# Performance work log

Measured on AMD Instinct MI355X. Metric: run time of the kernel, lower is better.

Reference implementation:

```python
import jax, jax.numpy as jnp
import numpy as np

MAX_EMBED = 1024
MAX_HEADS = 16
MIN_WIDTH_RATIO = 0.25


def setup_inputs() -> dict:
    key = jax.random.key(0)
    ks = jax.random.split(key, 10)
    B, S, E = 4, 1024, MAX_EMBED
    query = jax.random.normal(ks[0], (B, S, E), dtype=jnp.float32)
    attention_mask = jax.random.randint(ks[1], (B, 1, 1, S), 0, 2, dtype=jnp.int32)
    # SlimmableLinear params (max sizes); kaiming-ish scale ~ 1/sqrt(fan_in)
    scale = 1.0 / np.sqrt(E)
    def lin(kw, kb):
        w = jax.random.uniform(kw, (E, E), dtype=jnp.float32, minval=-scale, maxval=scale)
        b = jax.random.uniform(kb, (E,), dtype=jnp.float32, minval=-scale, maxval=scale)
        return w, b
    q_w, q_b = lin(ks[2], ks[3])
    k_w, k_b = lin(ks[4], ks[5])
    v_w, v_b = lin(ks[6], ks[7])
    o_w, o_b = lin(ks[8], ks[9])
    return {"query": query, "attention_mask": attention_mask,
            "q_w": q_w, "q_b": q_b, "k_w": k_w, "k_b": k_b,
            "v_w": v_w, "v_b": v_b, "o_w": o_w, "o_b": o_b,
            "width": 768}


def _slim_linear(x, w, b, width):
    # weight stored [out, in] like torch; slice to [width, width]
    return x[..., :width] @ w[:width, :width].T + b[:width]


def reference(query, attention_mask, q_w, q_b, k_w, k_b, v_w, v_b, o_w, o_b, width):
    min_width = int(MAX_EMBED * MIN_WIDTH_RATIO)
    width = max(min_width, min(int(width), MAX_EMBED))
    num_heads = max(1, width * MAX_HEADS // MAX_EMBED)
    head_dim = width // num_heads
    B, S, _ = query.shape

    q = _slim_linear(query, q_w, q_b, width)  # [B,S,width]
    k = _slim_linear(query, k_w, k_b, width)  # key=query (self-attn)
    v = _slim_linear(query, v_w, v_b, width)

    q = q.reshape(B, S, num_heads, head_dim).transpose(0, 2, 1, 3)  # [B,H,S,D]
    k = k.reshape(B, S, num_heads, head_dim).transpose(0, 2, 1, 3)
    v = v.reshape(B, S, num_heads, head_dim).transpose(0, 2, 1, 3)

    scores = jnp.einsum('bhqd,bhkd->bhqk', q, k) / jnp.sqrt(jnp.float32(head_dim))
    scores = jnp.where(attention_mask == 0, jnp.float32(-1e9), scores)
    attn_weights = jax.nn.softmax(scores, axis=-1)  # [B,H,S,S]
    attn_output = jnp.einsum('bhqk,bhkd->bhqd', attn_weights, v)
    attn_output = attn_output.transpose(0, 2, 1, 3).reshape(B, S, width)
    output = attn_output @ o_w[:width, :width].T + o_b[:width]
    return output, attn_weights
```

## Files before the change

### kernel.cpp

```cpp
#include <hip/hip_runtime.h>

#define Bn 4
#define Sn 1024
#define En 1024
#define Wn 768
#define Hn 12
#define Dn 64
#define XE ((size_t)Bn * Sn * Wn)

typedef __attribute__((ext_vector_type(8))) short short8;
typedef __attribute__((ext_vector_type(4))) short short4v;
typedef __attribute__((ext_vector_type(4))) float floatx4;

#define MFMA16(A, B, C) __builtin_amdgcn_mfma_f32_16x16x32_bf16(A, B, C, 0, 0, 0)

__device__ __forceinline__ unsigned short f2bf_rn(float f) {
    unsigned int u = __float_as_uint(f);
    unsigned int r = u + 0x7fffu + ((u >> 16) & 1u);
    return (unsigned short)(r >> 16);
}
__device__ __forceinline__ float bf2f(unsigned short h) {
    return __uint_as_float(((unsigned int)h) << 16);
}

__device__ __forceinline__ void gload_lds16(const unsigned short* g, unsigned short* l) {
    __builtin_amdgcn_global_load_lds(
        (const __attribute__((address_space(1))) void*)g,
        (__attribute__((address_space(3))) void*)l, 16, 0, 0);
}

__global__ __launch_bounds__(256) void prep_kernel(
    const float* __restrict__ x,
    const float* __restrict__ qw, const float* __restrict__ kw,
    const float* __restrict__ vw, const float* __restrict__ ow,
    const float* __restrict__ qb, const float* __restrict__ kb,
    const float* __restrict__ vb,
    unsigned short* __restrict__ xh, unsigned short* __restrict__ xl,
    unsigned short* __restrict__ wqh, unsigned short* __restrict__ wql,
    unsigned short* __restrict__ woh, unsigned short* __restrict__ wol,
    float* __restrict__ bq)
{
    const int bx = blockIdx.x;
    const float* src; unsigned short *dh, *dl; int e;
    if (bx < 3072) {
        e = (bx * 256 + threadIdx.x) * 4;
        src = x; dh = xh; dl = xl;
    } else if (bx < 3072 + 1728) {
        int bb = bx - 3072; int which = bb / 576;
        e = ((bb - which * 576) * 256 + threadIdx.x) * 4;
        src = (which == 0) ? qw : (which == 1) ? kw : vw;
        dh = wqh + (size_t)which * Wn * Wn;
        dl = wql + (size_t)which * Wn * Wn;
    } else if (bx < 3072 + 1728 + 576) {
        e = ((bx - 3072 - 1728) * 256 + threadIdx.x) * 4;
        src = ow; dh = woh; dl = wol;
    } else {
        int t = (bx - 3072 - 1728 - 576) * 256 + threadIdx.x;
        if (t < Wn) bq[t] = qb[t];
        else if (t < 2 * Wn) bq[t] = kb[t - Wn];
        else if (t < 3 * Wn) bq[t] = vb[t - 2 * Wn];
        return;
    }
    int row = e / Wn, col = e - row * Wn;
    float4 v = *(const float4*)(src + (size_t)row * En + col);
    float f[4] = {v.x, v.y, v.z, v.w};
    short4v h, l;
    #pragma unroll
    for (int i = 0; i < 4; ++i) {
        unsigned short hh = f2bf_rn(f[i]);
        h[i] = (short)hh;
        l[i] = (short)f2bf_rn(f[i] - bf2f(hh));
    }
    *(short4v*)(dh + e) = h;
    *(short4v*)(dl + e) = l;
}

__global__ __launch_bounds__(256) void qkv_mfma_kernel(
    const unsigned short* __restrict__ xh, const unsigned short* __restrict__ xl,
    const unsigned short* __restrict__ wh, const unsigned short* __restrict__ wl,
    const float* __restrict__ bq,
    unsigned short* __restrict__ qh_o, unsigned short* __restrict__ kh_o,
    unsigned short* __restrict__ vt_o)
{
    __shared__ __align__(16) unsigned short Ah[128 * 32];
    __shared__ __align__(16) unsigned short Al[128 * 32];
    __shared__ __align__(16) unsigned short Bh[128 * 32];
    __shared__ __align__(16) unsigned short Bl[128 * 32];

    const int tid = threadIdx.x;
    const int wave = tid >> 6, lane = tid & 63;
    const int quad = lane >> 4, l16 = lane & 15;
    const int m0 = blockIdx.x * 128, n0 = blockIdx.y * 128;
    const int wm = wave >> 1, wn = wave & 1;
    const int which = n0 / Wn;
    const bool full = (which == 2);

    floatx4 acc[4][4] = {};

    const unsigned short* gsrc = (wave == 0) ? xh : (wave == 1) ? xl
                               : (wave == 2) ? wh : wl;
    unsigned short* ldst = (wave == 0) ? Ah : (wave == 1) ? Al
                         : (wave == 2) ? Bh : Bl;
    const int base_row = (wave < 2) ? m0 : n0;
    const int r_in = lane >> 2;
    const int cs = (lane & 3) ^ (r_in & 3);

    for (int k0 = 0; k0 < Wn; k0 += 32) {
        if (full || wave == 0 || wave == 2) {
            #pragma unroll
            for (int i = 0; i < 8; ++i) {
                int r = i * 16 + r_in;
                const unsigned short* gp =
                    gsrc + (size_t)(base_row + r) * Wn + k0 + cs * 8;
                gload_lds16(gp, ldst + i * 512);
            }
        }
        __syncthreads();

        short8 afh[4], afl[4], bfh[4], bfl[4];
        #pragma unroll
        for (int t = 0; t < 4; ++t) {
            int mr = wm * 64 + t * 16 + l16;
            int ca = quad ^ (mr & 3);
            afh[t] = *(const short8*)(Ah + mr * 32 + ca * 8);
            if (full) afl[t] = *(const short8*)(Al + mr * 32 + ca * 8);
            int nr = wn * 64 + t * 16 + l16;
            int cb = quad ^ (nr & 3);
            bfh[t] = *(const short8*)(Bh + nr * 32 + cb * 8);
            if (full) bfl[t] = *(const short8*)(Bl + nr * 32 + cb * 8);
        }
        #pragma unroll
        for (int mt = 0; mt < 4; ++mt)
            #pragma unroll
            for (int nt = 0; nt < 4; ++nt) {
                acc[mt][nt] = MFMA16(afh[mt], bfh[nt], acc[mt][nt]);
                if (full) {
                    acc[mt][nt] = MFMA16(afh[mt], bfl[nt], acc[mt][nt]);
                    acc[mt][nt] = MFMA16(afl[mt], bfh[nt], acc[mt][nt]);
                }
            }
        __syncthreads();
    }

    const int b = m0 >> 10;
    #pragma unroll
    for (int nt = 0; nt < 4; ++nt) {
        const int ng = n0 + wn * 64 + nt * 16 + l16;
        const float bias = bq[ng];
        const int f = ng - which * Wn;
        const int h = f >> 6, d = f & 63;
        #pragma unroll
        for (int mt = 0; mt < 4; ++mt) {
            const int mbase = m0 + wm * 64 + mt * 16 + quad * 4;
            const int s0 = mbase & (Sn - 1);
            if (which < 2) {
                unsigned short* oq = which ? kh_o : qh_o;
                size_t idx = (((size_t)(b * Hn + h)) * Sn + s0) * Dn + d;
                #pragma unroll
                for (int r = 0; r < 4; ++r)
                    oq[idx + (size_t)r * Dn] = f2bf_rn(acc[mt][nt][r] + bias);
            } else {
                size_t idx = (((size_t)(b * Hn + h)) * Dn + d) * Sn + s0;
                short4v pk;
                #pragma unroll
                for (int r = 0; r < 4; ++r)
                    pk[r] = (short)f2bf_rn(acc[mt][nt][r] + bias);
                *(short4v*)(vt_o + idx) = pk;
            }
        }
    }
}

__global__ __launch_bounds__(256) void attn_sum_kernel(
    const unsigned short* __restrict__ qh, const unsigned short* __restrict__ kh,
    const int* __restrict__ mask, float* __restrict__ lpart)
{
    __shared__ float msk[256];

    const int tid = threadIdx.x;
    const int wave = tid >> 6, lane = tid & 63;
    const int quad = lane >> 4, l16 = lane & 15;
    const int qt = blockIdx.x >> 2, ks = blockIdx.x & 3;
    const int h = blockIdx.y, b = blockIdx.z;
    const int bh = b * Hn + h;
    const size_t kvb = (size_t)bh * Sn * Dn;

    if (tid < 64) {
        int4 mi = *(const int4*)(mask + b * Sn + ks * 256 + tid * 4);
        msk[tid * 4 + 0] = (float)mi.x;
        msk[tid * 4 + 1] = (float)mi.y;
        msk[tid * 4 + 2] = (float)mi.z;
        msk[tid * 4 + 3] = (float)mi.w;
    }

    short8 qf[2];
    {
        const int s = qt * 64 + wave * 16 + l16;
        const unsigned short* qp = qh + kvb + (size_t)s * Dn + quad * 8;
        qf[0] = *(const short8*)(qp);
        qf[1] = *(const short8*)(qp + 32);
    }
    __syncthreads();

    float lsum[4] = {0.f, 0.f, 0.f, 0.f};

    for (int kt = 0; kt < 4; ++kt) {
        #pragma unroll
        for (int ct = 0; ct < 4; ++ct) {
            const int kl = kt * 64 + ct * 16 + l16;
            const unsigned short* kp = kh + kvb + (size_t)(ks * 256 + kl) * Dn + quad * 8;
            short8 kf0 = *(const short8*)(kp);
            short8 kf1 = *(const short8*)(kp + 32);
            floatx4 acc = {0.f, 0.f, 0.f, 0.f};
            acc = MFMA16(qf[0], kf0, acc);
            acc = MFMA16(qf[1], kf1, acc);
            const float mv = msk[kl];
            #pragma unroll
            for (int r = 0; r < 4; ++r)
                lsum[r] += __expf(acc[r] * 0.125f) * mv;
        }
    }

    #pragma unroll
    for (int r = 0; r < 4; ++r) {
        float v = lsum[r];
        v += __shfl_xor(v, 1, 64);
        v += __shfl_xor(v, 2, 64);
        v += __shfl_xor(v, 4, 64);
        v += __shfl_xor(v, 8, 64);
        lsum[r] = v;
    }
    if (l16 == 0) {
        const int row = qt * 64 + wave * 16 + quad * 4;
        #pragma unroll
        for (int r = 0; r < 4; ++r)
            lpart[((size_t)ks * Bn * Hn + bh) * Sn + row + r] = lsum[r];
    }
}

__global__ __launch_bounds__(256) void attn_out_kernel(
    const unsigned short* __restrict__ qh, const unsigned short* __restrict__ kh,
    const unsigned short* __restrict__ vt, const int* __restrict__ mask,
    const float* __restrict__ lpart, float* __restrict__ attn,
    unsigned short* __restrict__ aoh, unsigned short* __restrict__ aol)
{
    __shared__ __align__(16) unsigned short Ps[4][16 * 72];
    __shared__ float msk[Sn];

    const int tid = threadIdx.x;
    const int wave = tid >> 6, lane = tid & 63;
    const int quad = lane >> 4, l16 = lane & 15;
    const int qt = blockIdx.x;
    const int h = blockIdx.y, b = blockIdx.z;
    const int bh = b * Hn + h;
    const size_t kvb = (size_t)bh * Sn * Dn;
    const size_t vbase = (size_t)bh * Dn * Sn;

    {
        int4 mi = *(const int4*)(mask + b * Sn + tid * 4);
        msk[tid * 4 + 0] = (float)mi.x;
        msk[tid * 4 + 1] = (float)mi.y;
        msk[tid * 4 + 2] = (float)mi.z;
        msk[tid * 4 + 3] = (float)mi.w;
    }

    short8 qf[2];
    {
        const int s = qt * 64 + wave * 16 + l16;
        const unsigned short* qp = qh + kvb + (size_t)s * Dn + quad * 8;
        qf[0] = *(const short8*)(qp);
        qf[1] = *(const short8*)(qp + 32);
    }

    const int row0 = qt * 64 + wave * 16 + quad * 4;
    float li[4];
    #pragma unroll
    for (int r = 0; r < 4; ++r) {
        float lv = 0.f;
        #pragma unroll
        for (int s4 = 0; s4 < 4; ++s4)
            lv += lpart[((size_t)s4 * Bn * Hn + bh) * Sn + row0 + r];
        li[r] = (lv > 0.f) ? 1.f / lv : 0.f;
    }
    __syncthreads();

    floatx4 oacc[4] = {};
    float* aprow = attn + ((size_t)bh * Sn + qt * 64 + wave * 16 + l16) * Sn;

    for (int kk = 0; kk < 16; ++kk) {
        const int k0 = kk * 64;
        #pragma unroll
        for (int ct = 0; ct < 4; ++ct) {
            const int key = k0 + ct * 16 + l16;
            const unsigned short* kp = kh + kvb + (size_t)key * Dn + quad * 8;
            short8 kf0 = *(const short8*)(kp);
            short8 kf1 = *(const short8*)(kp + 32);
            floatx4 acc = {0.f, 0.f, 0.f, 0.f};
            acc = MFMA16(qf[0], kf0, acc);
            acc = MFMA16(qf[1], kf1, acc);
            const float mv = msk[key];
            #pragma unroll
            for (int r = 0; r < 4; ++r) {
                const float p = __expf(acc[r] * 0.125f) * mv * li[r];
                Ps[wave][(quad * 4 + r) * 72 + ct * 16 + l16] = f2bf_rn(p);
            }
        }
        #pragma unroll
        for (int ksp = 0; ksp < 2; ++ksp) {
            short8 pf = *(const short8*)&Ps[wave][l16 * 72 + ksp * 32 + quad * 8];
            float4 f0, f1;
            f0.x = bf2f((unsigned short)pf[0]); f0.y = bf2f((unsigned short)pf[1]);
            f0.z = bf2f((unsigned short)pf[2]); f0.w = bf2f((unsigned short)pf[3]);
            f1.x = bf2f((unsigned short)pf[4]); f1.y = bf2f((unsigned short)pf[5]);
            f1.z = bf2f((unsigned short)pf[6]); f1.w = bf2f((unsigned short)pf[7]);
            float* ap = aprow + k0 + ksp * 32 + quad * 8;
            *(float4*)(ap)     = f0;
            *(float4*)(ap + 4) = f1;
            #pragma unroll
            for (int dt = 0; dt < 4; ++dt) {
                short8 vf = *(const short8*)(vt + vbase
                              + (size_t)(dt * 16 + l16) * Sn + k0 + ksp * 32 + quad * 8);
                oacc[dt] = MFMA16(pf, vf, oacc[dt]);
            }
        }
    }

    #pragma unroll
    for (int dt = 0; dt < 4; ++dt) {
        #pragma unroll
        for (int r = 0; r < 4; ++r) {
            const float o = oacc[dt][r];
            const unsigned short hh = f2bf_rn(o);
            const size_t idx = ((size_t)b * Sn + row0 + r) * Wn + h * Dn + dt * 16 + l16;
            aoh[idx] = hh;
            aol[idx] = f2bf_rn(o - bf2f(hh));
        }
    }
}

__global__ __launch_bounds__(256) void oproj_mfma_kernel(
    const unsigned short* __restrict__ aoh, const unsigned short* __restrict__ aol,
    const unsigned short* __restrict__ wh, const unsigned short* __restrict__ wl,
    const float* __restrict__ ob, float* __restrict__ out)
{
    __shared__ __align__(16) unsigned short Ah[64 * 32];
    __shared__ __align__(16) unsigned short Al[64 * 32];
    __shared__ __align__(16) unsigned short Bh[128 * 32];
    __shared__ __align__(16) unsigned short Bl[128 * 32];

    const int tid = threadIdx.x;
    const int wave = tid >> 6, lane = tid & 63;
    const int quad = lane >> 4, l16 = lane & 15;
    const int m0 = blockIdx.x * 64, n0 = blockIdx.y * 128;
    const int wm = wave >> 1, wn = wave & 1;

    floatx4 acc[2][4] = {};

    const int r_in = lane >> 2;
    const int cs = (lane & 3) ^ (r_in & 3);

    for (int k0 = 0; k0 < Wn; k0 += 32) {
        if (wave == 0) {
            #pragma unroll
            for (int i = 0; i < 4; ++i) {
                gload_lds16(aoh + (size_t)(m0 + i * 16 + r_in) * Wn + k0 + cs * 8,
                            Ah + i * 512);
                gload_lds16(aol + (size_t)(m0 + i * 16 + r_in) * Wn + k0 + cs * 8,
                            Al + i * 512);
            }
        } else if (wave == 1) {
            #pragma unroll
            for (int i = 0; i < 8; ++i)
                gload_lds16(wh + (size_t)(n0 + i * 16 + r_in) * Wn + k0 + cs * 8,
                            Bh + i * 512);
        } else if (wave == 2) {
            #pragma unroll
            for (int i = 0; i < 8; ++i)
                gload_lds16(wl + (size_t)(n0 + i * 16 + r_in) * Wn + k0 + cs * 8,
                            Bl + i * 512);
        }
        __syncthreads();

        short8 afh[2], afl[2], bfh[4], bfl[4];
        #pragma unroll
        for (int t = 0; t < 2; ++t) {
            int mr = wm * 32 + t * 16 + l16;
            int ca = quad ^ (mr & 3);
            afh[t] = *(const short8*)(Ah + mr * 32 + ca * 8);
            afl[t] = *(const short8*)(Al + mr * 32 + ca * 8);
        }
        #pragma unroll
        for (int t = 0; t < 4; ++t) {
            int nr = wn * 64 + t * 16 + l16;
            int cb = quad ^ (nr & 3);
            bfh[t] = *(const short8*)(Bh + nr * 32 + cb * 8);
            bfl[t] = *(const short8*)(Bl + nr * 32 + cb * 8);
        }
        #pragma unroll
        for (int mt = 0; mt < 2; ++mt)
            #pragma unroll
            for (int nt = 0; nt < 4; ++nt) {
                acc[mt][nt] = MFMA16(afh[mt], bfh[nt], acc[mt][nt]);
                acc[mt][nt] = MFMA16(afh[mt], bfl[nt], acc[mt][nt]);
                acc[mt][nt] = MFMA16(afl[mt], bfh[nt], acc[mt][nt]);
            }
        __syncthreads();
    }

    #pragma unroll
    for (int nt = 0; nt < 4; ++nt) {
        const int ng = n0 + wn * 64 + nt * 16 + l16;
        const float bias = ob[ng];
        #pragma unroll
        for (int mt = 0; mt < 2; ++mt) {
            const int m = m0 + wm * 32 + mt * 16 + quad * 4;
            #pragma unroll
            for (int r = 0; r < 4; ++r)
                out[(size_t)(m + r) * Wn + ng] = acc[mt][nt][r] + bias;
        }
    }
}

extern "C" void kernel_launch(void* const* d_in, const int* in_sizes, int n_in,
                              void* d_out, int out_size, void* d_ws, size_t ws_size,
                              hipStream_t stream) {
    const float* x    = (const float*)d_in[0];
    const int*   mask = (const int*)  d_in[1];
    const float* qw = (const float*)d_in[2];
    const float* qb = (const float*)d_in[3];
    const float* kw = (const float*)d_in[4];
    const float* kb = (const float*)d_in[5];
    const float* vw = (const float*)d_in[6];
    const float* vb = (const float*)d_in[7];
    const float* ow = (const float*)d_in[8];
    const float* ob = (const float*)d_in[9];

    float* out  = (float*)d_out;
    float* attn = out + XE;

    char* w = (char*)d_ws;
    unsigned short* xh   = (unsigned short*)w;  w += XE * 2;
    unsigned short* xl   = (unsigned short*)w;  w += XE * 2;
    unsigned short* wqh  = (unsigned short*)w;  w += (size_t)3 * Wn * Wn * 2;
    unsigned short* wql  = (unsigned short*)w;  w += (size_t)3 * Wn * Wn * 2;
    unsigned short* woh  = (unsigned short*)w;  w += (size_t)Wn * Wn * 2;
    unsigned short* wol  = (unsigned short*)w;  w += (size_t)Wn * Wn * 2;
    float*          bq   = (float*)w;           w += (size_t)3 * Wn * 4;
    unsigned short* qh   = (unsigned short*)w;  w += XE * 2;
    unsigned short* kh   = (unsigned short*)w;  w += XE * 2;
    unsigned short* vt_w = (unsigned short*)w;  w += XE * 2;
    float*          lpart = (float*)w;          w += (size_t)4 * Bn * Hn * Sn * 4;

    prep_kernel<<<5385, 256, 0, stream>>>(x, qw, kw, vw, ow, qb, kb, vb,
                                          xh, xl, wqh, wql, woh, wol, bq);

    qkv_mfma_kernel<<<dim3(32, 18), 256, 0, stream>>>(
        xh, xl, wqh, wql, bq, qh, kh, vt_w);

    attn_sum_kernel<<<dim3(64, Hn, Bn), 256, 0, stream>>>(
        qh, kh, mask, lpart);

    attn_out_kernel<<<dim3(16, Hn, Bn), 256, 0, stream>>>(
        qh, kh, vt_w, mask, lpart, attn, xh, xl);

    oproj_mfma_kernel<<<dim3(64, 6), 256, 0, stream>>>(
        xh, xl, woh, wol, ob, out);
}
```

Before: 444.9 us.

## Fuse attention row-sum and output passes into one kernel with register-held probabilities

The separate row-sum kernel and attention-output kernel become one 512-thread kernel. Each pair of waves splits the key range in half, keeps the unnormalised bf16 probabilities in registers, and exchanges row sums and partial PV accumulators through shared memory. This removes the second QK^T recompute, the lpart round trip and one launch. In exchange it uses 16 short8 registers per lane for the probabilities, which may raise register pressure and lower occupancy. Probabilities are now rounded to bf16 before normalisation, which slightly changes both the stored attention weights and the PV input.

```diff
diff --git a/kernel.cpp b/kernel.cpp
--- a/kernel.cpp
+++ b/kernel.cpp
@@ -171,92 +171,28 @@
     }
 }
 
-__global__ __launch_bounds__(256) void attn_sum_kernel(
+__global__ __launch_bounds__(512) void attn_fused_kernel(
     const unsigned short* __restrict__ qh, const unsigned short* __restrict__ kh,
-    const int* __restrict__ mask, float* __restrict__ lpart)
+    const unsigned short* __restrict__ vt, const int* __restrict__ mask,
+    float* __restrict__ attn,
+    unsigned short* __restrict__ aoh, unsigned short* __restrict__ aol)
 {
-    __shared__ float msk[256];
+    __shared__ __align__(16) unsigned short Ps[8][16 * 72];
+    __shared__ float msk[Sn];
+    __shared__ float Lsum[8][16];
+    __shared__ __align__(16) float Obuf[4][16][68];
 
     const int tid = threadIdx.x;
     const int wave = tid >> 6, lane = tid & 63;
     const int quad = lane >> 4, l16 = lane & 15;
-    const int qt = blockIdx.x >> 2, ks = blockIdx.x & 3;
-    const int h = blockIdx.y, b = blockIdx.z;
-    const int bh = b * Hn + h;
-    const size_t kvb = (size_t)bh * Sn * Dn;
-
-    if (tid < 64) {
-        int4 mi = *(const int4*)(mask + b * Sn + ks * 256 + tid * 4);
-        msk[tid * 4 + 0] = (float)mi.x;
-        msk[tid * 4 + 1] = (float)mi.y;
-        msk[tid * 4 + 2] = (float)mi.z;
-        msk[tid * 4 + 3] = (float)mi.w;
-    }
-
-    short8 qf[2];
-    {
-        const int s = qt * 64 + wave * 16 + l16;
-        const unsigned short* qp = qh + kvb + (size_t)s * Dn + quad * 8;
-        qf[0] = *(const short8*)(qp);
-        qf[1] = *(const short8*)(qp + 32);
-    }
-    __syncthreads();
-
-    float lsum[4] = {0.f, 0.f, 0.f, 0.f};
-
-    for (int kt = 0; kt < 4; ++kt) {
-        #pragma unroll
-        for (int ct = 0; ct < 4; ++ct) {
-            const int kl = kt * 64 + ct * 16 + l16;
-            const unsigned short* kp = kh + kvb + (size_t)(ks * 256 + kl) * Dn + quad * 8;
-            short8 kf0 = *(const short8*)(kp);
-            short8 kf1 = *(const short8*)(kp + 32);
-            floatx4 acc = {0.f, 0.f, 0.f, 0.f};
-            acc = MFMA16(qf[0], kf0, acc);
-            acc = MFMA16(qf[1], kf1, acc);
-            const float mv = msk[kl];
-            #pragma unroll
-            for (int r = 0; r < 4; ++r)
-                lsum[r] += __expf(acc[r] * 0.125f) * mv;
-        }
-    }
-
-    #pragma unroll
-    for (int r = 0; r < 4; ++r) {
-        float v = lsum[r];
-        v += __shfl_xor(v, 1, 64);
-        v += __shfl_xor(v, 2, 64);
-        v += __shfl_xor(v, 4, 64);
-        v += __shfl_xor(v, 8, 64);
-        lsum[r] = v;
-    }
-    if (l16 == 0) {
-        const int row = qt * 64 + wave * 16 + quad * 4;
-        #pragma unroll
-        for (int r = 0; r < 4; ++r)
-            lpart[((size_t)ks * Bn * Hn + bh) * Sn + row + r] = lsum[r];
-    }
-}
-
-__global__ __launch_bounds__(256) void attn_out_kernel(
-    const unsigned short* __restrict__ qh, const unsigned short* __restrict__ kh,
-    const unsigned short* __restrict__ vt, const int* __restrict__ mask,
-    const float* __restrict__ lpart, float* __restrict__ attn,
-    unsigned short* __restrict__ aoh, unsigned short* __restrict__ aol)
-{
-    __shared__ __align__(16) unsigned short Ps[4][16 * 72];
-    __shared__ float msk[Sn];
-
-    const int tid = threadIdx.x;
-    const int wave = tid >> 6, lane = tid & 63;
-    const int quad = lane >> 4, l16 = lane & 15;
+    const int pair = wave >> 1, hf = wave & 1;
     const int qt = blockIdx.x;
     const int h = blockIdx.y, b = blockIdx.z;
     const int bh = b * Hn + h;
     const size_t kvb = (size_t)bh * Sn * Dn;
     const size_t vbase = (size_t)bh * Dn * Sn;
 
-    {
+    if (tid < 256) {
         int4 mi = *(const int4*)(mask + b * Sn + tid * 4);
         msk[tid * 4 + 0] = (float)mi.x;
         msk[tid * 4 + 1] = (float)mi.y;
@@ -264,31 +200,22 @@
         msk[tid * 4 + 3] = (float)mi.w;
     }
 
+    const int qrow = qt * 64 + pair * 16 + l16;
     short8 qf[2];
     {
-        const int s = qt * 64 + wave * 16 + l16;
-        const unsigned short* qp = qh + kvb + (size_t)s * Dn + quad * 8;
+        const unsigned short* qp = qh + kvb + (size_t)qrow * Dn + quad * 8;
         qf[0] = *(const short8*)(qp);
         qf[1] = *(const short8*)(qp + 32);
     }
-
-    const int row0 = qt * 64 + wave * 16 + quad * 4;
-    float li[4];
-    #pragma unroll
-    for (int r = 0; r < 4; ++r) {
-        float lv = 0.f;
-        #pragma unroll
-        for (int s4 = 0; s4 < 4; ++s4)
-            lv += lpart[((size_t)s4 * Bn * Hn + bh) * Sn + row0 + r];
-        li[r] = (lv > 0.f) ? 1.f / lv : 0.f;
-    }
     __syncthreads();
 
-    floatx4 oacc[4] = {};
-    float* aprow = attn + ((size_t)bh * Sn + qt * 64 + wave * 16 + l16) * Sn;
-
-    for (int kk = 0; kk < 16; ++kk) {
-        const int k0 = kk * 64;
+    short8 Pr[16];
+    float lsumr[4] = {0.f, 0.f, 0.f, 0.f};
+    const int kbase = hf * 512;
+
+    #pragma unroll
+    for (int kk = 0; kk < 8; ++kk) {
+        const int k0 = kbase + kk * 64;
         #pragma unroll
         for (int ct = 0; ct < 4; ++ct) {
             const int key = k0 + ct * 16 + l16;
@@ -301,18 +228,60 @@
             const float mv = msk[key];
             #pragma unroll
             for (int r = 0; r < 4; ++r) {
-                const float p = __expf(acc[r] * 0.125f) * mv * li[r];
-                Ps[wave][(quad * 4 + r) * 72 + ct * 16 + l16] = f2bf_rn(p);
-            }
-        }
+                const float e = __expf(acc[r] * 0.125f) * mv;
+                lsumr[r] += e;
+                Ps[wave][(quad * 4 + r) * 72 + ct * 16 + l16] = f2bf_rn(e);
+            }
+        }
+        Pr[kk * 2 + 0] = *(const short8*)&Ps[wave][l16 * 72 + quad * 8];
+        Pr[kk * 2 + 1] = *(const short8*)&Ps[wave][l16 * 72 + 32 + quad * 8];
+    }
+
+    #pragma unroll
+    for (int r = 0; r < 4; ++r) {
+        float v = lsumr[r];
+        v += __shfl_xor(v, 1, 64);
+        v += __shfl_xor(v, 2, 64);
+        v += __shfl_xor(v, 4, 64);
+        v += __shfl_xor(v, 8, 64);
+        lsumr[r] = v;
+    }
+    if (l16 == 0) {
+        #pragma unroll
+        for (int r = 0; r < 4; ++r) Lsum[wave][quad * 4 + r] = lsumr[r];
+    }
+    __syncthreads();
+
+    float li[4];
+    #pragma unroll
+    for (int r = 0; r < 4; ++r) {
+        const float lv = Lsum[pair * 2][quad * 4 + r] + Lsum[pair * 2 + 1][quad * 4 + r];
+        li[r] = (lv > 0.f) ? 1.f / lv : 0.f;
+    }
+    float lt;
+    {
+        const float lv = Lsum[pair * 2][l16] + Lsum[pair * 2 + 1][l16];
+        lt = (lv > 0.f) ? 1.f / lv : 0.f;
+    }
+
+    floatx4 oacc[4] = {};
+    float* aprow = attn + ((size_t)bh * Sn + qrow) * Sn;
+
+    #pragma unroll
+    for (int kk = 0; kk < 8; ++kk) {
+        const int k0 = kbase + kk * 64;
         #pragma unroll
         for (int ksp = 0; ksp < 2; ++ksp) {
-            short8 pf = *(const short8*)&Ps[wave][l16 * 72 + ksp * 32 + quad * 8];
+            const short8 pf = Pr[kk * 2 + ksp];
             float4 f0, f1;
-            f0.x = bf2f((unsigned short)pf[0]); f0.y = bf2f((unsigned short)pf[1]);
-            f0.z = bf2f((unsigned short)pf[2]); f0.w = bf2f((unsigned short)pf[3]);
-            f1.x = bf2f((unsigned short)pf[4]); f1.y = bf2f((unsigned short)pf[5]);
-            f1.z = bf2f((unsigned short)pf[6]); f1.w = bf2f((unsigned short)pf[7]);
+            f0.x = bf2f((unsigned short)pf[0]) * lt;
+            f0.y = bf2f((unsigned short)pf[1]) * lt;
+            f0.z = bf2f((unsigned short)pf[2]) * lt;
+            f0.w = bf2f((unsigned short)pf[3]) * lt;
+            f1.x = bf2f((unsigned short)pf[4]) * lt;
+            f1.y = bf2f((unsigned short)pf[5]) * lt;
+            f1.z = bf2f((unsigned short)pf[6]) * lt;
+            f1.w = bf2f((unsigned short)pf[7]) * lt;
             float* ap = aprow + k0 + ksp * 32 + quad * 8;
             *(float4*)(ap)     = f0;
             *(float4*)(ap + 4) = f1;
@@ -325,16 +294,26 @@
         }
     }
 
-    #pragma unroll
-    for (int dt = 0; dt < 4; ++dt) {
-        #pragma unroll
-        for (int r = 0; r < 4; ++r) {
-            const float o = oacc[dt][r];
-            const unsigned short hh = f2bf_rn(o);
-            const size_t idx = ((size_t)b * Sn + row0 + r) * Wn + h * Dn + dt * 16 + l16;
-            aoh[idx] = hh;
-            aol[idx] = f2bf_rn(o - bf2f(hh));
-        }
+    if (hf == 1) {
+        #pragma unroll
+        for (int dt = 0; dt < 4; ++dt)
+            #pragma unroll
+            for (int r = 0; r < 4; ++r)
+                Obuf[pair][quad * 4 + r][dt * 16 + l16] = oacc[dt][r];
+    }
+    __syncthreads();
+    if (hf == 0) {
+        const int row0 = qt * 64 + pair * 16 + quad * 4;
+        #pragma unroll
+        for (int dt = 0; dt < 4; ++dt)
+            #pragma unroll
+            for (int r = 0; r < 4; ++r) {
+                const float o = (oacc[dt][r] + Obuf[pair][quad * 4 + r][dt * 16 + l16]) * li[r];
+                const unsigned short hh = f2bf_rn(o);
+                const size_t idx = ((size_t)b * Sn + row0 + r) * Wn + h * Dn + dt * 16 + l16;
+                aoh[idx] = hh;
+                aol[idx] = f2bf_rn(o - bf2f(hh));
+            }
     }
 }
 
@@ -449,7 +428,6 @@
     unsigned short* qh   = (unsigned short*)w;  w += XE * 2;
     unsigned short* kh   = (unsigned short*)w;  w += XE * 2;
     unsigned short* vt_w = (unsigned short*)w;  w += XE * 2;
-    float*          lpart = (float*)w;          w += (size_t)4 * Bn * Hn * Sn * 4;
 
     prep_kernel<<<5385, 256, 0, stream>>>(x, qw, kw, vw, ow, qb, kb, vb,
                                           xh, xl, wqh, wql, woh, wol, bq);
@@ -457,11 +435,8 @@
     qkv_mfma_kernel<<<dim3(32, 18), 256, 0, stream>>>(
         xh, xl, wqh, wql, bq, qh, kh, vt_w);
 
-    attn_sum_kernel<<<dim3(64, Hn, Bn), 256, 0, stream>>>(
-        qh, kh, mask, lpart);
-
-    attn_out_kernel<<<dim3(16, Hn, Bn), 256, 0, stream>>>(
-        qh, kh, vt_w, mask, lpart, attn, xh, xl);
+    attn_fused_kernel<<<dim3(16, Hn, Bn), 512, 0, stream>>>(
+        qh, kh, vt_w, mask, attn, xh, xl);
 
     oproj_mfma_kernel<<<dim3(64, 6), 256, 0, stream>>>(
         xh, xl, woh, wol, ob, out);
```

New measurement: 408.2 us. 8.3% less time.
